# Optimization experiments

Hardware: AMD Instinct MI355X
Metric: run time of the kernel (lower is better)

The kernel has to match this reference:

```python
import jax, jax.numpy as jnp
import numpy as np

SIGMA = 1.0

def setup_inputs() -> dict:
    key = jax.random.key(0)
    kx, ky = jax.random.split(key)
    x = jax.random.normal(kx, (8192, 256), dtype=jnp.float32)
    y = jax.random.normal(ky, (8192, 256), dtype=jnp.float32)
    return {"x": x, "y": y}

def reference(x, y):
    x2 = jnp.sum(x * x, axis=-1)            # [N]
    y2 = jnp.sum(y * y, axis=-1)            # [M]
    d2 = x2[:, None] + y2[None, :] - 2.0 * (x @ y.T)  # [N, M]
    d2 = jnp.maximum(d2, 0.0)
    k = jnp.exp(-d2 / (2.0 * SIGMA ** 2))
    # original: exp(...)[None].sum(dim=0).mean() == mean over all N*M entries
    return jnp.mean(k)
```

## Files before the change

kernel.cpp:

```cpp
#include <hip/hip_runtime.h>

#define NROWS 8192
#define DIM   256

typedef __bf16 bf16x8 __attribute__((ext_vector_type(8)));
typedef __bf16 bf16x4 __attribute__((ext_vector_type(4)));
typedef float  f32x4  __attribute__((ext_vector_type(4)));

typedef __attribute__((address_space(3))) char lds_char;
typedef __attribute__((address_space(1))) const char glob_char;

__global__ __launch_bounds__(256) void prep_kernel(
    const float* __restrict__ x, const float* __restrict__ y,
    __bf16* __restrict__ xb, __bf16* __restrict__ yb,
    float* __restrict__ x2, float* __restrict__ y2)
{
    int tid  = threadIdx.x;
    int lane = tid & 63;
    int w    = tid >> 6;
    int row  = blockIdx.x * 4 + w;
    bool isx = row < NROWS;
    int r    = isx ? row : row - NROWS;
    const float* src = (isx ? x : y) + (size_t)r * DIM;
    float4 v = reinterpret_cast<const float4*>(src)[lane];
    float sq = v.x*v.x + v.y*v.y + v.z*v.z + v.w*v.w;
    #pragma unroll
    for (int off = 32; off; off >>= 1) sq += __shfl_xor(sq, off);
    bf16x4 h;
    h[0] = (__bf16)v.x; h[1] = (__bf16)v.y; h[2] = (__bf16)v.z; h[3] = (__bf16)v.w;
    __bf16* dst = (isx ? xb : yb) + (size_t)r * DIM + lane * 4;
    *reinterpret_cast<bf16x4*>(dst) = h;
    if (lane == 0) (isx ? x2 : y2)[r] = sq;
}

__global__ void zero_kernel(float* out) {
    if (threadIdx.x == 0 && blockIdx.x == 0) out[0] = 0.0f;
}

__global__ __launch_bounds__(256) void rbf_gemm_kernel(
    const __bf16* __restrict__ xb, const __bf16* __restrict__ yb,
    const float* __restrict__ x2, const float* __restrict__ y2,
    float* __restrict__ out)
{
    __shared__ __bf16 Asm_[128 * 64];
    __shared__ __bf16 Bsm_[128 * 64];
    __shared__ float  red[4];

    int tid  = threadIdx.x;
    int lane = tid & 63;
    int wv   = tid >> 6;
    int wm   = wv >> 1, wn = wv & 1;
    int bm   = blockIdx.x & 63;
    int bn   = blockIdx.x >> 6;

    f32x4 acc[4][4];
    #pragma unroll
    for (int m = 0; m < 4; ++m)
        #pragma unroll
        for (int n = 0; n < 4; ++n)
            acc[m][n] = (f32x4){0.f, 0.f, 0.f, 0.f};

    int h   = lane >> 4;
    int l15 = lane & 15;

    for (int kt = 0; kt < 4; ++kt) {
        #pragma unroll
        for (int i = 0; i < 4; ++i) {
            int lin = i * 4096 + tid * 16;
            int row = lin >> 7;
            int kb  = lin & 127;
            int kbs = kb ^ ((row & 7) << 4);
            size_t gA = (size_t)(bm * 128 + row) * 512 + (size_t)kt * 128 + kbs;
            size_t gB = (size_t)(bn * 128 + row) * 512 + (size_t)kt * 128 + kbs;
            __builtin_amdgcn_global_load_lds(
                (glob_char*)((const char*)xb + gA),
                (lds_char*)((char*)Asm_ + i * 4096 + wv * 1024), 16, 0, 0);
            __builtin_amdgcn_global_load_lds(
                (glob_char*)((const char*)yb + gB),
                (lds_char*)((char*)Bsm_ + i * 4096 + wv * 1024), 16, 0, 0);
        }
        __syncthreads();

        #pragma unroll
        for (int kk = 0; kk < 2; ++kk) {
            bf16x8 af[4], bfr[4];
            #pragma unroll
            for (int m = 0; m < 4; ++m) {
                int row = wm * 64 + m * 16 + l15;
                int kb  = (kk * 64 + h * 16) ^ ((row & 7) << 4);
                af[m] = *reinterpret_cast<const bf16x8*>((const char*)Asm_ + row * 128 + kb);
            }
            #pragma unroll
            for (int n = 0; n < 4; ++n) {
                int row = wn * 64 + n * 16 + l15;
                int kb  = (kk * 64 + h * 16) ^ ((row & 7) << 4);
                bfr[n] = *reinterpret_cast<const bf16x8*>((const char*)Bsm_ + row * 128 + kb);
            }
            #pragma unroll
            for (int m = 0; m < 4; ++m)
                #pragma unroll
                for (int n = 0; n < 4; ++n)
                    acc[m][n] = __builtin_amdgcn_mfma_f32_16x16x32_bf16(
                        af[m], bfr[n], acc[m][n], 0, 0, 0);
        }
        __syncthreads();
    }

    float lsum = 0.f;
    int colbase = bn * 128 + wn * 64 + l15;
    int rowbase = bm * 128 + wm * 64 + h * 4;
    float y2v[4];
    #pragma unroll
    for (int n = 0; n < 4; ++n) y2v[n] = y2[colbase + n * 16];
    #pragma unroll
    for (int m = 0; m < 4; ++m) {
        #pragma unroll
        for (int r = 0; r < 4; ++r) {
            float xr = x2[rowbase + m * 16 + r];
            #pragma unroll
            for (int n = 0; n < 4; ++n) {
                float d2 = fmaf(-2.0f, acc[m][n][r], xr + y2v[n]);
                d2 = fmaxf(d2, 0.0f);
                lsum += exp2f(d2 * -0.7213475204444817f);
            }
        }
    }
    #pragma unroll
    for (int off = 32; off; off >>= 1) lsum += __shfl_xor(lsum, off);
    if (lane == 0) red[wv] = lsum;
    __syncthreads();
    if (tid == 0) {
        float s = (red[0] + red[1] + red[2] + red[3]) * 1.4901161193847656e-08f;
        atomicAdd(out, s);
    }
}

extern "C" void kernel_launch(void* const* d_in, const int* in_sizes, int n_in,
                              void* d_out, int out_size, void* d_ws, size_t ws_size,
                              hipStream_t stream) {
    const float* x = (const float*)d_in[0];
    const float* y = (const float*)d_in[1];
    float* out = (float*)d_out;
    char* ws = (char*)d_ws;
    __bf16* xb = (__bf16*)ws;
    __bf16* yb = (__bf16*)(ws + (size_t)4 * 1024 * 1024);
    float*  x2 = (float*)(ws + (size_t)8 * 1024 * 1024);
    float*  y2 = (float*)(ws + (size_t)8 * 1024 * 1024 + 32 * 1024);

    hipLaunchKernelGGL(zero_kernel, dim3(1), dim3(64), 0, stream, out);
    hipLaunchKernelGGL(prep_kernel, dim3(4096), dim3(256), 0, stream,
                       x, y, xb, yb, x2, y2);
    hipLaunchKernelGGL(rbf_gemm_kernel, dim3(4096), dim3(256), 0, stream,
                       xb, yb, x2, y2, out);
}
```

Measured before the change: 131.1 us.

## Use 256x256 tiles with double-buffered LDS and fold exponent constants into prep

The GEMM tile grows from 128x128 with 4 waves to 256x256 with 8 waves, and a 128KB double-buffered LDS prefetches the next K slice while MFMAs run on the current one. Prep now stores -0.5*log2e*||x||^2 so the epilogue collapses to one fma plus exp2, and the clamp at zero is dropped. The separate zero kernel is folded into prep. The large LDS footprint limits occupancy to one block per CU. Dropping the clamp can change results slightly when rounding makes d2 negative, though the clamp mostly matters in degenerate cases.

```diff
diff --git a/kernel.cpp b/kernel.cpp
--- a/kernel.cpp
+++ b/kernel.cpp
@@ -10,10 +10,14 @@
 typedef __attribute__((address_space(3))) char lds_char;
 typedef __attribute__((address_space(1))) const char glob_char;
 
+#define LOG2E  1.4426950408889634f
+#define NEG_HALF_LOG2E (-0.7213475204444817f)
+
 __global__ __launch_bounds__(256) void prep_kernel(
     const float* __restrict__ x, const float* __restrict__ y,
     __bf16* __restrict__ xb, __bf16* __restrict__ yb,
-    float* __restrict__ x2, float* __restrict__ y2)
+    float* __restrict__ px, float* __restrict__ py,
+    float* __restrict__ out)
 {
     int tid  = threadIdx.x;
     int lane = tid & 63;
@@ -30,99 +34,105 @@
     h[0] = (__bf16)v.x; h[1] = (__bf16)v.y; h[2] = (__bf16)v.z; h[3] = (__bf16)v.w;
     __bf16* dst = (isx ? xb : yb) + (size_t)r * DIM + lane * 4;
     *reinterpret_cast<bf16x4*>(dst) = h;
-    if (lane == 0) (isx ? x2 : y2)[r] = sq;
+    if (lane == 0) (isx ? px : py)[r] = NEG_HALF_LOG2E * sq;
+    if (blockIdx.x == 0 && tid == 0) out[0] = 0.0f;
 }
 
-__global__ void zero_kernel(float* out) {
-    if (threadIdx.x == 0 && blockIdx.x == 0) out[0] = 0.0f;
-}
-
-__global__ __launch_bounds__(256) void rbf_gemm_kernel(
+__global__ __launch_bounds__(512, 1) void rbf_gemm_kernel(
     const __bf16* __restrict__ xb, const __bf16* __restrict__ yb,
-    const float* __restrict__ x2, const float* __restrict__ y2,
+    const float* __restrict__ px, const float* __restrict__ py,
     float* __restrict__ out)
 {
-    __shared__ __bf16 Asm_[128 * 64];
-    __shared__ __bf16 Bsm_[128 * 64];
-    __shared__ float  red[4];
+    __shared__ char smem[131072];
+    __shared__ float red[8];
 
     int tid  = threadIdx.x;
     int lane = tid & 63;
     int wv   = tid >> 6;
-    int wm   = wv >> 1, wn = wv & 1;
-    int bm   = blockIdx.x & 63;
-    int bn   = blockIdx.x >> 6;
+    int wm   = wv >> 2;
+    int wn   = wv & 3;
+    int bm   = blockIdx.x & 31;
+    int bn   = blockIdx.x >> 5;
+    int h    = lane >> 4;
+    int l15  = lane & 15;
 
-    f32x4 acc[4][4];
+    f32x4 acc[8][4];
     #pragma unroll
-    for (int m = 0; m < 4; ++m)
+    for (int m = 0; m < 8; ++m)
         #pragma unroll
         for (int n = 0; n < 4; ++n)
             acc[m][n] = (f32x4){0.f, 0.f, 0.f, 0.f};
 
-    int h   = lane >> 4;
-    int l15 = lane & 15;
-
-    for (int kt = 0; kt < 4; ++kt) {
+    auto stage = [&](int buf, int kt) {
+        size_t ktoff = (size_t)kt * 128;
         #pragma unroll
         for (int i = 0; i < 4; ++i) {
-            int lin = i * 4096 + tid * 16;
+            int lin = i * 8192 + tid * 16;
             int row = lin >> 7;
-            int kb  = lin & 127;
-            int kbs = kb ^ ((row & 7) << 4);
-            size_t gA = (size_t)(bm * 128 + row) * 512 + (size_t)kt * 128 + kbs;
-            size_t gB = (size_t)(bn * 128 + row) * 512 + (size_t)kt * 128 + kbs;
+            int kbs = (lin & 127) ^ ((row & 7) << 4);
+            size_t gA = (size_t)(bm * 256 + row) * 512 + ktoff + kbs;
+            size_t gB = (size_t)(bn * 256 + row) * 512 + ktoff + kbs;
+            int ldsoff = buf * 65536 + i * 8192 + wv * 1024;
             __builtin_amdgcn_global_load_lds(
                 (glob_char*)((const char*)xb + gA),
-                (lds_char*)((char*)Asm_ + i * 4096 + wv * 1024), 16, 0, 0);
+                (lds_char*)(smem + ldsoff), 16, 0, 0);
             __builtin_amdgcn_global_load_lds(
                 (glob_char*)((const char*)yb + gB),
-                (lds_char*)((char*)Bsm_ + i * 4096 + wv * 1024), 16, 0, 0);
+                (lds_char*)(smem + 32768 + ldsoff), 16, 0, 0);
         }
-        __syncthreads();
+    };
 
+    auto compute = [&](int buf) {
+        const char* Ab = smem + buf * 65536;
+        const char* Bb = Ab + 32768;
         #pragma unroll
         for (int kk = 0; kk < 2; ++kk) {
-            bf16x8 af[4], bfr[4];
-            #pragma unroll
-            for (int m = 0; m < 4; ++m) {
-                int row = wm * 64 + m * 16 + l15;
-                int kb  = (kk * 64 + h * 16) ^ ((row & 7) << 4);
-                af[m] = *reinterpret_cast<const bf16x8*>((const char*)Asm_ + row * 128 + kb);
-            }
+            bf16x8 af[8], bfr[4];
             #pragma unroll
             for (int n = 0; n < 4; ++n) {
                 int row = wn * 64 + n * 16 + l15;
                 int kb  = (kk * 64 + h * 16) ^ ((row & 7) << 4);
-                bfr[n] = *reinterpret_cast<const bf16x8*>((const char*)Bsm_ + row * 128 + kb);
+                bfr[n] = *reinterpret_cast<const bf16x8*>(Bb + row * 128 + kb);
             }
             #pragma unroll
-            for (int m = 0; m < 4; ++m)
+            for (int m = 0; m < 8; ++m) {
+                int row = wm * 128 + m * 16 + l15;
+                int kb  = (kk * 64 + h * 16) ^ ((row & 7) << 4);
+                af[m] = *reinterpret_cast<const bf16x8*>(Ab + row * 128 + kb);
+            }
+            #pragma unroll
+            for (int m = 0; m < 8; ++m)
                 #pragma unroll
                 for (int n = 0; n < 4; ++n)
                     acc[m][n] = __builtin_amdgcn_mfma_f32_16x16x32_bf16(
                         af[m], bfr[n], acc[m][n], 0, 0, 0);
         }
+    };
+
+    stage(0, 0);
+    __syncthreads();
+    #pragma unroll
+    for (int kt = 0; kt < 4; ++kt) {
+        int cur = kt & 1;
+        if (kt < 3) stage(cur ^ 1, kt + 1);
+        compute(cur);
         __syncthreads();
     }
 
     float lsum = 0.f;
-    int colbase = bn * 128 + wn * 64 + l15;
-    int rowbase = bm * 128 + wm * 64 + h * 4;
-    float y2v[4];
+    int colbase = bn * 256 + wn * 64 + l15;
+    int rowbase = bm * 256 + wm * 128 + h * 4;
+    float py4[4];
     #pragma unroll
-    for (int n = 0; n < 4; ++n) y2v[n] = y2[colbase + n * 16];
+    for (int n = 0; n < 4; ++n) py4[n] = py[colbase + n * 16];
     #pragma unroll
-    for (int m = 0; m < 4; ++m) {
+    for (int m = 0; m < 8; ++m) {
         #pragma unroll
         for (int r = 0; r < 4; ++r) {
-            float xr = x2[rowbase + m * 16 + r];
+            float pxv = px[rowbase + m * 16 + r];
             #pragma unroll
-            for (int n = 0; n < 4; ++n) {
-                float d2 = fmaf(-2.0f, acc[m][n][r], xr + y2v[n]);
-                d2 = fmaxf(d2, 0.0f);
-                lsum += exp2f(d2 * -0.7213475204444817f);
-            }
+            for (int n = 0; n < 4; ++n)
+                lsum += exp2f(fmaf(acc[m][n][r], LOG2E, pxv + py4[n]));
         }
     }
     #pragma unroll
@@ -130,7 +140,8 @@
     if (lane == 0) red[wv] = lsum;
     __syncthreads();
     if (tid == 0) {
-        float s = (red[0] + red[1] + red[2] + red[3]) * 1.4901161193847656e-08f;
+        float s = (red[0] + red[1] + red[2] + red[3] +
+                   red[4] + red[5] + red[6] + red[7]) * 1.4901161193847656e-08f;
         atomicAdd(out, s);
     }
 }
@@ -144,12 +155,11 @@
     char* ws = (char*)d_ws;
     __bf16* xb = (__bf16*)ws;
     __bf16* yb = (__bf16*)(ws + (size_t)4 * 1024 * 1024);
-    float*  x2 = (float*)(ws + (size_t)8 * 1024 * 1024);
-    float*  y2 = (float*)(ws + (size_t)8 * 1024 * 1024 + 32 * 1024);
+    float*  px = (float*)(ws + (size_t)8 * 1024 * 1024);
+    float*  py = (float*)(ws + (size_t)8 * 1024 * 1024 + 32 * 1024);
 
-    hipLaunchKernelGGL(zero_kernel, dim3(1), dim3(64), 0, stream, out);
     hipLaunchKernelGGL(prep_kernel, dim3(4096), dim3(256), 0, stream,
-                       x, y, xb, yb, x2, y2);
-    hipLaunchKernelGGL(rbf_gemm_kernel, dim3(4096), dim3(256), 0, stream,
-                       xb, yb, x2, y2, out);
+                       x, y, xb, yb, px, py, out);
+    hipLaunchKernelGGL(rbf_gemm_kernel, dim3(1024), dim3(512), 0, stream,
+                       xb, yb, px, py, out);
 }
```

Result: faster. 115.7 us (-11.7%).
